# Performance work log

Measured on AMD Instinct MI355X. Metric: run time of the kernel, lower is better.

The kernel has to match this reference:

```python
import jax, jax.numpy as jnp
import numpy as np

IN_FEATURES = 1024
OUT_FEATURES = 4096
HARMONICS = 32
TOKENS = 16384


def setup_inputs() -> dict:
    key = jax.random.key(0)
    k_x, k_basis, k_phase = jax.random.split(key, 3)
    x = jax.random.normal(k_x, (TOKENS, IN_FEATURES), dtype=jnp.float32)
    basis = jax.random.normal(k_basis, (HARMONICS, IN_FEATURES), dtype=jnp.float32)
    # F.normalize(basis, p=2, dim=1)
    basis = basis / jnp.linalg.norm(basis, axis=1, keepdims=True)
    two_pi = 2.0 * np.pi
    phase = jax.random.normal(k_phase, (OUT_FEATURES, HARMONICS), dtype=jnp.float32) * two_pi
    amp = jnp.ones((OUT_FEATURES, HARMONICS), dtype=jnp.float32) / HARMONICS
    return {"x": x, "basis": basis, "phase": phase, "amp": amp}


def reference(x, basis, phase, amp):
    # resonance = F.linear(x, basis): [T, H]
    resonance = jnp.einsum("ti,hi->th", x, basis)
    # wave is complex(resonance, 0); resonator = amp * exp(i*phase).
    # real((wave * resonator).sum(-1)) == resonance @ (amp*cos(phase))^T since wave.imag == 0.
    w_real = amp * jnp.cos(phase)  # [O, H]
    return jnp.einsum("th,oh->to", resonance, w_real)
```

## Files before the change

kernel.cpp:

```cpp
#include <hip/hip_runtime.h>

#define T_TOK 16384
#define IN_F  1024
#define OUT_F 4096
#define NH    32

__global__ __launch_bounds__(256) void wreal_kernel(
    const float* __restrict__ phase, const float* __restrict__ amp,
    float* __restrict__ w_t)
{
    int idx = blockIdx.x * 256 + threadIdx.x;
    int o = idx & (OUT_F - 1);
    int h = idx >> 12;
    float p = phase[o * NH + h];
    float a = amp[o * NH + h];
    w_t[h * OUT_F + o] = a * cosf(p);
}

#define G1_TT 64
#define G1_KC 128
#define G1_S  132

__global__ __launch_bounds__(256) void resonance_kernel(
    const float* __restrict__ x,
    const float* __restrict__ basis,
    float* __restrict__ res_t)
{
    __shared__ float xs[G1_TT * G1_S];
    __shared__ float bs[NH * G1_S];

    const int tid = threadIdx.x;
    const int t0  = blockIdx.x * G1_TT;
    const int ty  = tid >> 4;
    const int tx  = tid & 15;

    float acc[4][2] = {};

    for (int i0 = 0; i0 < IN_F; i0 += G1_KC) {
        #pragma unroll
        for (int it = 0; it < 8; ++it) {
            int lin = it * 256 + tid;
            int r = lin >> 5, c = lin & 31;
            float4 v = *(const float4*)(x + (size_t)(t0 + r) * IN_F + i0 + 4 * c);
            *(float4*)(xs + r * G1_S + 4 * c) = v;
        }
        #pragma unroll
        for (int it = 0; it < 4; ++it) {
            int lin = it * 256 + tid;
            int r = lin >> 5, c = lin & 31;
            float4 v = *(const float4*)(basis + (size_t)r * IN_F + i0 + 4 * c);
            *(float4*)(bs + r * G1_S + 4 * c) = v;
        }
        __syncthreads();

        #pragma unroll 4
        for (int i = 0; i < G1_KC; i += 4) {
            float4 xa[4], bb[2];
            #pragma unroll
            for (int k = 0; k < 4; ++k)
                xa[k] = *(const float4*)(xs + (4 * ty + k) * G1_S + i);
            #pragma unroll
            for (int j = 0; j < 2; ++j)
                bb[j] = *(const float4*)(bs + (tx + 16 * j) * G1_S + i);
            #pragma unroll
            for (int k = 0; k < 4; ++k) {
                #pragma unroll
                for (int j = 0; j < 2; ++j) {
                    acc[k][j] += xa[k].x * bb[j].x;
                    acc[k][j] += xa[k].y * bb[j].y;
                    acc[k][j] += xa[k].z * bb[j].z;
                    acc[k][j] += xa[k].w * bb[j].w;
                }
            }
        }
        __syncthreads();
    }

    #pragma unroll
    for (int k = 0; k < 4; ++k)
        #pragma unroll
        for (int j = 0; j < 2; ++j)
            res_t[(size_t)(tx + 16 * j) * T_TOK + t0 + 4 * ty + k] = acc[k][j];
}

#define G2_TT 64
#define G2_OT 128
#define RS_S  68
#define WT_S  132

__global__ __launch_bounds__(256) void holo_out_kernel(
    const float* __restrict__ res_t,
    const float* __restrict__ w_t,
    float* __restrict__ out)
{
    __shared__ float rs[NH * RS_S];
    __shared__ float wl[NH * WT_S];

    const int tid = threadIdx.x;
    const int o0  = blockIdx.x * G2_OT;
    const int t0  = blockIdx.y * G2_TT;
    const int ty  = tid >> 4;
    const int tx  = tid & 15;

    #pragma unroll
    for (int it = 0; it < 2; ++it) {
        int lin = it * 256 + tid;
        int r = lin >> 4, c = lin & 15;
        float4 v = *(const float4*)(res_t + (size_t)r * T_TOK + t0 + 4 * c);
        *(float4*)(rs + r * RS_S + 4 * c) = v;
    }
    #pragma unroll
    for (int it = 0; it < 4; ++it) {
        int lin = it * 256 + tid;
        int r = lin >> 5, c = lin & 31;
        float4 v = *(const float4*)(w_t + (size_t)r * OUT_F + o0 + 4 * c);
        *(float4*)(wl + r * WT_S + 4 * c) = v;
    }
    __syncthreads();

    float acc[4][8] = {};
    #pragma unroll
    for (int h = 0; h < NH; ++h) {
        float4 rt = *(const float4*)(rs + h * RS_S + 4 * ty);
        float4 wa = *(const float4*)(wl + h * WT_S + 4 * tx);
        float4 wb = *(const float4*)(wl + h * WT_S + 64 + 4 * tx);
        float r4[4] = {rt.x, rt.y, rt.z, rt.w};
        float w8[8] = {wa.x, wa.y, wa.z, wa.w, wb.x, wb.y, wb.z, wb.w};
        #pragma unroll
        for (int k = 0; k < 4; ++k)
            #pragma unroll
            for (int j = 0; j < 8; ++j)
                acc[k][j] += r4[k] * w8[j];
    }

    #pragma unroll
    for (int k = 0; k < 4; ++k) {
        float* po = out + (size_t)(t0 + 4 * ty + k) * OUT_F + o0;
        *(float4*)(po + 4 * tx)      = make_float4(acc[k][0], acc[k][1], acc[k][2], acc[k][3]);
        *(float4*)(po + 64 + 4 * tx) = make_float4(acc[k][4], acc[k][5], acc[k][6], acc[k][7]);
    }
}

extern "C" void kernel_launch(void* const* d_in, const int* in_sizes, int n_in,
                              void* d_out, int out_size, void* d_ws, size_t ws_size,
                              hipStream_t stream)
{
    const float* x     = (const float*)d_in[0];
    const float* basis = (const float*)d_in[1];
    const float* phase = (const float*)d_in[2];
    const float* amp   = (const float*)d_in[3];
    float* out = (float*)d_out;

    float* res_t = (float*)d_ws;
    float* w_t   = res_t + (size_t)NH * T_TOK;

    wreal_kernel<<<dim3((OUT_F * NH) / 256), dim3(256), 0, stream>>>(phase, amp, w_t);
    resonance_kernel<<<dim3(T_TOK / G1_TT), dim3(256), 0, stream>>>(x, basis, res_t);
    holo_out_kernel<<<dim3(OUT_F / G2_OT, T_TOK / G2_TT), dim3(256), 0, stream>>>(res_t, w_t, out);
}
```

Baseline: 354.8 us.

## Split-K resonance GEMM with atomics and register-resident weights in output kernel

The first GEMM now splits the 1024-wide reduction four ways across a second grid dimension and accumulates partial sums with atomicAdd into a token-major buffer, which the wreal kernel zeroes first. This raises the block count for the skinny x·basisᵀ stage. The output kernel drops shared memory: each thread holds 32 float4 weight columns in registers and streams tokens, reading resonance rows via broadcast loads. The cost is atomic traffic, non-deterministic summation order, and heavy register use in the output kernel.

Result: slower. 529.8 us (+49.3%).

```diff
diff --git a/kernel.cpp b/kernel.cpp
--- a/kernel.cpp
+++ b/kernel.cpp
@@ -7,7 +7,7 @@
 
 __global__ __launch_bounds__(256) void wreal_kernel(
     const float* __restrict__ phase, const float* __restrict__ amp,
-    float* __restrict__ w_t)
+    float* __restrict__ w_t, float4* __restrict__ res0)
 {
     int idx = blockIdx.x * 256 + threadIdx.x;
     int o = idx & (OUT_F - 1);
@@ -15,129 +15,109 @@
     float p = phase[o * NH + h];
     float a = amp[o * NH + h];
     w_t[h * OUT_F + o] = a * cosf(p);
+    res0[idx] = make_float4(0.f, 0.f, 0.f, 0.f);
 }
 
-#define G1_TT 64
-#define G1_KC 128
-#define G1_S  132
+#define G1_KC 64
+#define KSPLIT 4
+#define XS 68
 
 __global__ __launch_bounds__(256) void resonance_kernel(
     const float* __restrict__ x,
     const float* __restrict__ basis,
-    float* __restrict__ res_t)
+    float* __restrict__ res)
 {
-    __shared__ float xs[G1_TT * G1_S];
-    __shared__ float bs[NH * G1_S];
+    __shared__ float xs[64 * XS];
+    __shared__ float bs[NH * XS];
 
     const int tid = threadIdx.x;
-    const int t0  = blockIdx.x * G1_TT;
-    const int ty  = tid >> 4;
-    const int tx  = tid & 15;
+    const int t0  = blockIdx.x * 64;
+    const int kb  = blockIdx.y;
+    const int ty  = tid & 31;
+    const int th  = tid >> 5;
 
-    float acc[4][2] = {};
+    float acc[2][4] = {};
 
-    for (int i0 = 0; i0 < IN_F; i0 += G1_KC) {
-        #pragma unroll
-        for (int it = 0; it < 8; ++it) {
-            int lin = it * 256 + tid;
-            int r = lin >> 5, c = lin & 31;
-            float4 v = *(const float4*)(x + (size_t)(t0 + r) * IN_F + i0 + 4 * c);
-            *(float4*)(xs + r * G1_S + 4 * c) = v;
-        }
+    for (int kk = 0; kk < IN_F / KSPLIT; kk += G1_KC) {
+        const int i0 = kb * (IN_F / KSPLIT) + kk;
         #pragma unroll
         for (int it = 0; it < 4; ++it) {
             int lin = it * 256 + tid;
-            int r = lin >> 5, c = lin & 31;
+            int r = lin >> 4, c = lin & 15;
+            float4 v = *(const float4*)(x + (size_t)(t0 + r) * IN_F + i0 + 4 * c);
+            *(float4*)(xs + r * XS + 4 * c) = v;
+        }
+        #pragma unroll
+        for (int it = 0; it < 2; ++it) {
+            int lin = it * 256 + tid;
+            int r = lin >> 4, c = lin & 15;
             float4 v = *(const float4*)(basis + (size_t)r * IN_F + i0 + 4 * c);
-            *(float4*)(bs + r * G1_S + 4 * c) = v;
+            *(float4*)(bs + r * XS + 4 * c) = v;
         }
         __syncthreads();
 
-        #pragma unroll 4
+        #pragma unroll
         for (int i = 0; i < G1_KC; i += 4) {
-            float4 xa[4], bb[2];
+            float4 xa0 = *(const float4*)(xs + ty * XS + i);
+            float4 xa1 = *(const float4*)(xs + (ty + 32) * XS + i);
+            float4 bb[4];
             #pragma unroll
-            for (int k = 0; k < 4; ++k)
-                xa[k] = *(const float4*)(xs + (4 * ty + k) * G1_S + i);
+            for (int j = 0; j < 4; ++j)
+                bb[j] = *(const float4*)(bs + (4 * th + j) * XS + i);
             #pragma unroll
-            for (int j = 0; j < 2; ++j)
-                bb[j] = *(const float4*)(bs + (tx + 16 * j) * G1_S + i);
-            #pragma unroll
-            for (int k = 0; k < 4; ++k) {
-                #pragma unroll
-                for (int j = 0; j < 2; ++j) {
-                    acc[k][j] += xa[k].x * bb[j].x;
-                    acc[k][j] += xa[k].y * bb[j].y;
-                    acc[k][j] += xa[k].z * bb[j].z;
-                    acc[k][j] += xa[k].w * bb[j].w;
-                }
+            for (int j = 0; j < 4; ++j) {
+                acc[0][j] += xa0.x * bb[j].x;
+                acc[0][j] += xa0.y * bb[j].y;
+                acc[0][j] += xa0.z * bb[j].z;
+                acc[0][j] += xa0.w * bb[j].w;
+                acc[1][j] += xa1.x * bb[j].x;
+                acc[1][j] += xa1.y * bb[j].y;
+                acc[1][j] += xa1.z * bb[j].z;
+                acc[1][j] += xa1.w * bb[j].w;
             }
         }
         __syncthreads();
     }
 
     #pragma unroll
-    for (int k = 0; k < 4; ++k)
-        #pragma unroll
-        for (int j = 0; j < 2; ++j)
-            res_t[(size_t)(tx + 16 * j) * T_TOK + t0 + 4 * ty + k] = acc[k][j];
+    for (int j = 0; j < 4; ++j) {
+        atomicAdd(res + (size_t)(t0 + ty) * NH + 4 * th + j, acc[0][j]);
+        atomicAdd(res + (size_t)(t0 + ty + 32) * NH + 4 * th + j, acc[1][j]);
+    }
 }
 
-#define G2_TT 64
-#define G2_OT 128
-#define RS_S  68
-#define WT_S  132
+#define TC3 64
 
-__global__ __launch_bounds__(256) void holo_out_kernel(
-    const float* __restrict__ res_t,
+__global__ __launch_bounds__(256, 2) void holo_out_kernel(
+    const float* __restrict__ res,
     const float* __restrict__ w_t,
     float* __restrict__ out)
 {
-    __shared__ float rs[NH * RS_S];
-    __shared__ float wl[NH * WT_S];
+    const int tid = threadIdx.x;
+    const int o   = blockIdx.x * 1024 + tid * 4;
+    const int t0  = blockIdx.y * TC3;
 
-    const int tid = threadIdx.x;
-    const int o0  = blockIdx.x * G2_OT;
-    const int t0  = blockIdx.y * G2_TT;
-    const int ty  = tid >> 4;
-    const int tx  = tid & 15;
+    float4 w4[NH];
+    #pragma unroll
+    for (int h = 0; h < NH; ++h)
+        w4[h] = *(const float4*)(w_t + (size_t)h * OUT_F + o);
 
-    #pragma unroll
-    for (int it = 0; it < 2; ++it) {
-        int lin = it * 256 + tid;
-        int r = lin >> 4, c = lin & 15;
-        float4 v = *(const float4*)(res_t + (size_t)r * T_TOK + t0 + 4 * c);
-        *(float4*)(rs + r * RS_S + 4 * c) = v;
-    }
-    #pragma unroll
-    for (int it = 0; it < 4; ++it) {
-        int lin = it * 256 + tid;
-        int r = lin >> 5, c = lin & 31;
-        float4 v = *(const float4*)(w_t + (size_t)r * OUT_F + o0 + 4 * c);
-        *(float4*)(wl + r * WT_S + 4 * c) = v;
-    }
-    __syncthreads();
-
-    float acc[4][8] = {};
-    #pragma unroll
-    for (int h = 0; h < NH; ++h) {
-        float4 rt = *(const float4*)(rs + h * RS_S + 4 * ty);
-        float4 wa = *(const float4*)(wl + h * WT_S + 4 * tx);
-        float4 wb = *(const float4*)(wl + h * WT_S + 64 + 4 * tx);
-        float r4[4] = {rt.x, rt.y, rt.z, rt.w};
-        float w8[8] = {wa.x, wa.y, wa.z, wa.w, wb.x, wb.y, wb.z, wb.w};
+    for (int t = t0; t < t0 + TC3; t += 2) {
+        const float* r0 = res + (size_t)t * NH;
+        const float* r1 = r0 + NH;
+        float4 a0 = make_float4(0.f, 0.f, 0.f, 0.f);
+        float4 a1 = make_float4(0.f, 0.f, 0.f, 0.f);
         #pragma unroll
-        for (int k = 0; k < 4; ++k)
-            #pragma unroll
-            for (int j = 0; j < 8; ++j)
-                acc[k][j] += r4[k] * w8[j];
-    }
-
-    #pragma unroll
-    for (int k = 0; k < 4; ++k) {
-        float* po = out + (size_t)(t0 + 4 * ty + k) * OUT_F + o0;
-        *(float4*)(po + 4 * tx)      = make_float4(acc[k][0], acc[k][1], acc[k][2], acc[k][3]);
-        *(float4*)(po + 64 + 4 * tx) = make_float4(acc[k][4], acc[k][5], acc[k][6], acc[k][7]);
+        for (int h = 0; h < NH; ++h) {
+            float s0 = r0[h];
+            float s1 = r1[h];
+            a0.x += s0 * w4[h].x; a0.y += s0 * w4[h].y;
+            a0.z += s0 * w4[h].z; a0.w += s0 * w4[h].w;
+            a1.x += s1 * w4[h].x; a1.y += s1 * w4[h].y;
+            a1.z += s1 * w4[h].z; a1.w += s1 * w4[h].w;
+        }
+        *(float4*)(out + (size_t)t * OUT_F + o)       = a0;
+        *(float4*)(out + (size_t)(t + 1) * OUT_F + o) = a1;
     }
 }
 
@@ -151,10 +131,13 @@
     const float* amp   = (const float*)d_in[3];
     float* out = (float*)d_out;
 
-    float* res_t = (float*)d_ws;
-    float* w_t   = res_t + (size_t)NH * T_TOK;
+    float* res = (float*)d_ws;
+    float* w_t = res + (size_t)T_TOK * NH;
 
-    wreal_kernel<<<dim3((OUT_F * NH) / 256), dim3(256), 0, stream>>>(phase, amp, w_t);
-    resonance_kernel<<<dim3(T_TOK / G1_TT), dim3(256), 0, stream>>>(x, basis, res_t);
-    holo_out_kernel<<<dim3(OUT_F / G2_OT, T_TOK / G2_TT), dim3(256), 0, stream>>>(res_t, w_t, out);
+    wreal_kernel<<<dim3((OUT_F * NH) / 256), dim3(256), 0, stream>>>(
+        phase, amp, w_t, (float4*)res);
+    resonance_kernel<<<dim3(T_TOK / 64, KSPLIT), dim3(256), 0, stream>>>(
+        x, basis, res);
+    holo_out_kernel<<<dim3(OUT_F / 1024, T_TOK / TC3), dim3(256), 0, stream>>>(
+        res, w_t, out);
 }
```
